# Kernel tuning notes

Measured on AMD Instinct MI355X. Metric: run time of the kernel, lower is better.

The kernel has to match this reference:

```python
import jax, jax.numpy as jnp
import numpy as np

B, S, H, HD, WIN, KS = 2, 2048, 8, 64, 64, 2048
D = H * HD          # slotsize = nheads * headsize = 512
SUB = 1 + 2 * WIN   # window length = 129
LN_EPS = 1e-3       # Keras LayerNormalization default epsilon


def setup_inputs() -> dict:
    key = jax.random.key(0)
    ks = jax.random.split(key, 5)
    s = 0.02
    return {
        "values": jax.random.normal(ks[0], (B, S, D), jnp.float32),
        "W_kqv": jax.random.normal(ks[1], (D, 3 * D), jnp.float32) * s,
        "b_kqv": jnp.zeros((3 * D,), jnp.float32),
        "ln_gamma": jnp.ones((D,), jnp.float32),
        "ln_beta": jnp.zeros((D,), jnp.float32),
        "W_kernel": jax.random.normal(ks[2], (D, KS), jnp.float32) * s,
        "b_kernel": jnp.zeros((KS,), jnp.float32),
        "W_proj": jax.random.normal(ks[3], (KS, D), jnp.float32) * s,
        "b_proj": jnp.zeros((D,), jnp.float32),
    }


def _layernorm(x, g, b):
    mu = jnp.mean(x, axis=-1, keepdims=True)
    var = jnp.var(x, axis=-1, keepdims=True)
    return (x - mu) * jax.lax.rsqrt(var + LN_EPS) * g + b


def reference(values, W_kqv, b_kqv, ln_gamma, ln_beta, W_kernel, b_kernel, W_proj, b_proj):
    # fused qkv projection: [B,S,3D]
    kqv = values @ W_kqv + b_kqv
    k, q, v = jnp.split(kqv, 3, axis=2)
    # shared layernorm applied to q and k (over full D)
    q = _layernorm(q, ln_gamma, ln_beta)
    k = _layernorm(k, ln_gamma, ln_beta)
    kh = k.reshape(B, S, H, HD)
    qh = q.reshape(B, S, H, HD)
    vh = v.reshape(B, S, H, HD)
    starts = jnp.clip(jnp.arange(S) - WIN, 0, S - SUB)
    idx = starts[:, None] + jnp.arange(SUB)          # [S, SUB]
    kw = kh[:, idx]                                  # [B,S,SUB,H,HD]
    vw = vh[:, idx]                                  # [B,S,SUB,H,HD]
    scores = jnp.einsum('bshd,bswhd->bshw', qh, kw) / np.float32(np.sqrt(HD))
    attn = jax.nn.softmax(scores, axis=-1)           # [B,S,H,SUB]
    ctx = jnp.einsum('bshw,bswhd->bshd', attn, vw).reshape(B, S, D)
    # residual MLP (dropout rate 0 -> identity)
    x = jax.nn.relu(ctx @ W_kernel + b_kernel)
    x = x @ W_proj + b_proj
    return x + v  # residual is the value projection, per the original code
```

## Files before the change

### kernel.cpp

```cpp
#include <hip/hip_runtime.h>
#include <hip/hip_bf16.h>

#define B_ 2
#define S_ 2048
#define H_ 8
#define HD_ 64
#define WIN_ 64
#define SUB_ 129
#define D_ 512
#define KS_ 2048
#define M_ 4096
#define LN_EPS 1e-3f

typedef unsigned short u16;
typedef short bf16x8 __attribute__((ext_vector_type(8)));
typedef float f32x4 __attribute__((ext_vector_type(4)));

__device__ inline u16 f2bf(float x) {
  unsigned int u = __float_as_uint(x);
  return (u16)((u + 0x7fffu + ((u >> 16) & 1u)) >> 16);
}
__device__ inline float bf2f(u16 u) {
  return __uint_as_float(((unsigned int)u) << 16);
}
__device__ inline float bf2f_lo(unsigned int u) { return __uint_as_float(u << 16); }
__device__ inline float bf2f_hi(unsigned int u) { return __uint_as_float(u & 0xffff0000u); }

__device__ inline void gll16(const u16* g, u16* l) {
  __builtin_amdgcn_global_load_lds(
      (const __attribute__((address_space(1))) void*)g,
      (__attribute__((address_space(3))) void*)l, 16, 0, 0);
}

template <int EPI>
__global__ __launch_bounds__(256) void mfma_gemm(
    const u16* __restrict__ A, const u16* __restrict__ Bt,
    const float* __restrict__ bias, u16* __restrict__ Cout,
    float* __restrict__ stats, int K, int lda, int ldb, int ldc, int TN) {
  __shared__ __align__(16) u16 As[2][8192];
  __shared__ __align__(16) u16 Bs[2][8192];

  const int tid = threadIdx.x;
  const int wv = tid >> 6;
  const int ln = tid & 63;

  const int id = blockIdx.x;
  const int xcd = id & 7;
  const int sub = id >> 3;
  const int tn = sub % TN;
  const int msub = sub / TN;
  const int row0 = (xcd * 4 + msub) << 7;
  const int col0 = tn << 7;

  const int lrow = ln >> 3;
  const int lchunk = (ln & 7) ^ lrow;
  const u16* ag = A + (size_t)(row0 + 32 * wv + lrow) * lda + lchunk * 8;
  const u16* bg = Bt + (size_t)(col0 + 32 * wv + lrow) * ldb + lchunk * 8;
  const int lbase = 32 * wv * 64;

  const int quad = ln >> 4;
  const int l15 = ln & 15;
  const int r7 = l15 & 7;
  const int wm = (wv & 1) << 6;
  const int wn = (wv >> 1) << 6;

  f32x4 acc[4][4];
#pragma unroll
  for (int i = 0; i < 4; ++i)
#pragma unroll
    for (int j = 0; j < 4; ++j) acc[i][j] = (f32x4){0.f, 0.f, 0.f, 0.f};

#define STAGE(buf, koff)                                            \
  do {                                                              \
    const u16* a0 = ag + (koff);                                    \
    const u16* b0 = bg + (koff);                                    \
    u16* la = &As[buf][lbase];                                      \
    u16* lb = &Bs[buf][lbase];                                      \
    gll16(a0, la);                                                  \
    gll16(a0 + 8 * (size_t)lda, la + 512);                          \
    gll16(a0 + 16 * (size_t)lda, la + 1024);                       \
    gll16(a0 + 24 * (size_t)lda, la + 1536);                       \
    gll16(b0, lb);                                                  \
    gll16(b0 + 8 * (size_t)ldb, lb + 512);                          \
    gll16(b0 + 16 * (size_t)ldb, lb + 1024);                       \
    gll16(b0 + 24 * (size_t)ldb, lb + 1536);                       \
  } while (0)

  const int nk = K >> 6;
  STAGE(0, 0);

  for (int ki = 0; ki < nk; ++ki) {
    __syncthreads();
    if (ki + 1 < nk) STAGE((ki + 1) & 1, (ki + 1) << 6);

    const char* Ab = (const char*)As[ki & 1];
    const char* Bb = (const char*)Bs[ki & 1];
#pragma unroll
    for (int ks = 0; ks < 2; ++ks) {
      const int pc = ((quad + 4 * ks) ^ r7) << 4;
      bf16x8 af[4], bfv[4];
#pragma unroll
      for (int mi = 0; mi < 4; ++mi)
        af[mi] = *(const bf16x8*)(Ab + (wm + 16 * mi + l15) * 128 + pc);
#pragma unroll
      for (int ni = 0; ni < 4; ++ni)
        bfv[ni] = *(const bf16x8*)(Bb + (wn + 16 * ni + l15) * 128 + pc);
#pragma unroll
      for (int mi = 0; mi < 4; ++mi)
#pragma unroll
        for (int ni = 0; ni < 4; ++ni)
          acc[mi][ni] = __builtin_amdgcn_mfma_f32_16x16x32_bf16(
              bfv[ni], af[mi], acc[mi][ni], 0, 0, 0);
    }
  }
#undef STAGE

  const int c00 = col0 + wn + (quad << 2);
  float4 bv[4];
#pragma unroll
  for (int ni = 0; ni < 4; ++ni) bv[ni] = *(const float4*)&bias[c00 + ni * 16];

#pragma unroll
  for (int mi = 0; mi < 4; ++mi) {
    const int row = row0 + wm + 16 * mi + l15;
    float s = 0.f, ss = 0.f;
#pragma unroll
    for (int ni = 0; ni < 4; ++ni) {
      float v0 = acc[mi][ni][0] + bv[ni].x;
      float v1 = acc[mi][ni][1] + bv[ni].y;
      float v2 = acc[mi][ni][2] + bv[ni].z;
      float v3 = acc[mi][ni][3] + bv[ni].w;
      if (EPI == 1) {
        v0 = fmaxf(v0, 0.f); v1 = fmaxf(v1, 0.f);
        v2 = fmaxf(v2, 0.f); v3 = fmaxf(v3, 0.f);
      }
      if (EPI == 3) {
        s += v0 + v1 + v2 + v3;
        ss += v0 * v0 + v1 * v1 + v2 * v2 + v3 * v3;
      }
      ushort4 o = {f2bf(v0), f2bf(v1), f2bf(v2), f2bf(v3)};
      *(ushort4*)&Cout[(size_t)row * ldc + c00 + ni * 16] = o;
    }
    if (EPI == 3) {
      s += __shfl_xor(s, 16); ss += __shfl_xor(ss, 16);
      s += __shfl_xor(s, 32); ss += __shfl_xor(ss, 32);
      if (quad == 0 && col0 < 1024) {
        const int half = col0 >> 9;
        atomicAdd(&stats[(size_t)row * 4 + half * 2 + 0], s);
        atomicAdd(&stats[(size_t)row * 4 + half * 2 + 1], ss);
      }
    }
  }
}

__global__ __launch_bounds__(256) void mfma_gemm64(
    const u16* __restrict__ A, const u16* __restrict__ Bt,
    const float* __restrict__ bias, const u16* __restrict__ extra,
    float* __restrict__ Cout, int K, int lda, int ldb, int ldc, int eld) {
  __shared__ __align__(16) u16 As[2][4096];
  __shared__ __align__(16) u16 Bs[2][4096];

  const int tid = threadIdx.x;
  const int wv = tid >> 6;
  const int ln = tid & 63;

  const int id = blockIdx.x;
  const int xcd = id & 7;
  const int sub = id >> 3;
  const int tn = sub & 7;
  const int msub = sub >> 3;
  const int row0 = (xcd * 8 + msub) << 6;
  const int col0 = tn << 6;

  const int lrow = ln >> 3;
  const int lchunk = (ln & 7) ^ lrow;
  const u16* ag = A + (size_t)(row0 + 16 * wv + lrow) * lda + lchunk * 8;
  const u16* bg = Bt + (size_t)(col0 + 16 * wv + lrow) * ldb + lchunk * 8;
  const int lbase = 16 * wv * 64;

  const int quad = ln >> 4;
  const int l15 = ln & 15;
  const int r7 = l15 & 7;
  const int wm = (wv & 1) << 5;
  const int wn = (wv >> 1) << 5;

  f32x4 acc[2][2];
#pragma unroll
  for (int i = 0; i < 2; ++i)
#pragma unroll
    for (int j = 0; j < 2; ++j) acc[i][j] = (f32x4){0.f, 0.f, 0.f, 0.f};

#define STAGE64(buf, koff)                                          \
  do {                                                              \
    const u16* a0 = ag + (koff);                                    \
    const u16* b0 = bg + (koff);                                    \
    u16* la = &As[buf][lbase];                                      \
    u16* lb = &Bs[buf][lbase];                                      \
    gll16(a0, la);                                                  \
    gll16(a0 + 8 * (size_t)lda, la + 512);                          \
    gll16(b0, lb);                                                  \
    gll16(b0 + 8 * (size_t)ldb, lb + 512);                          \
  } while (0)

  const int nk = K >> 6;
  STAGE64(0, 0);

  for (int ki = 0; ki < nk; ++ki) {
    __syncthreads();
    if (ki + 1 < nk) STAGE64((ki + 1) & 1, (ki + 1) << 6);

    const char* Ab = (const char*)As[ki & 1];
    const char* Bb = (const char*)Bs[ki & 1];
#pragma unroll
    for (int ks = 0; ks < 2; ++ks) {
      const int pc = ((quad + 4 * ks) ^ r7) << 4;
      bf16x8 af[2], bfv[2];
#pragma unroll
      for (int mi = 0; mi < 2; ++mi)
        af[mi] = *(const bf16x8*)(Ab + (wm + 16 * mi + l15) * 128 + pc);
#pragma unroll
      for (int ni = 0; ni < 2; ++ni)
        bfv[ni] = *(const bf16x8*)(Bb + (wn + 16 * ni + l15) * 128 + pc);
#pragma unroll
      for (int mi = 0; mi < 2; ++mi)
#pragma unroll
        for (int ni = 0; ni < 2; ++ni)
          acc[mi][ni] = __builtin_amdgcn_mfma_f32_16x16x32_bf16(
              bfv[ni], af[mi], acc[mi][ni], 0, 0, 0);
    }
  }
#undef STAGE64

  const int c00 = col0 + wn + (quad << 2);
  float4 bv[2];
#pragma unroll
  for (int ni = 0; ni < 2; ++ni) bv[ni] = *(const float4*)&bias[c00 + ni * 16];

#pragma unroll
  for (int mi = 0; mi < 2; ++mi) {
    const int row = row0 + wm + 16 * mi + l15;
#pragma unroll
    for (int ni = 0; ni < 2; ++ni) {
      const int c = c00 + ni * 16;
      uint2 ex = *(const uint2*)&extra[(size_t)row * eld + c];
      float4 o;
      o.x = acc[mi][ni][0] + bv[ni].x + bf2f_lo(ex.x);
      o.y = acc[mi][ni][1] + bv[ni].y + bf2f_hi(ex.x);
      o.z = acc[mi][ni][2] + bv[ni].z + bf2f_lo(ex.y);
      o.w = acc[mi][ni][3] + bv[ni].w + bf2f_hi(ex.y);
      *(float4*)&Cout[(size_t)row * ldc + c] = o;
    }
  }
}

__global__ __launch_bounds__(256) void fused_cvt(
    const float* __restrict__ values, u16* __restrict__ vals_bf,
    const float* __restrict__ Wkqv, u16* __restrict__ wkqv_t,
    const float* __restrict__ Wker, u16* __restrict__ wker_t,
    const float* __restrict__ Wproj, u16* __restrict__ wproj_t,
    float* __restrict__ stats) {
  __shared__ float t[32][33];
  const int id = blockIdx.x;
  if (id >= 3840) {
    const int i = ((id - 3840) * 256 + threadIdx.x) * 4;
    *(float4*)&stats[i] = (float4){0.f, 0.f, 0.f, 0.f};
    return;
  }
  if (id < 1024) {
    const int i = (id * 256 + threadIdx.x) * 8;
    float4 a = *(const float4*)&values[i];
    float4 b = *(const float4*)&values[i + 4];
    union { u16 u[8]; uint4 v; } pk;
    pk.u[0] = f2bf(a.x); pk.u[1] = f2bf(a.y); pk.u[2] = f2bf(a.z); pk.u[3] = f2bf(a.w);
    pk.u[4] = f2bf(b.x); pk.u[5] = f2bf(b.y); pk.u[6] = f2bf(b.z); pk.u[7] = f2bf(b.w);
    *(uint4*)&vals_bf[i] = pk.v;
    return;
  }
  const float* W; u16* Wt; int K, N, nx, lin;
  if (id < 1792)      { lin = id - 1024; W = Wkqv;  Wt = wkqv_t;  K = 512;  N = 1536; nx = 48; }
  else if (id < 2816) { lin = id - 1792; W = Wker;  Wt = wker_t;  K = 512;  N = 2048; nx = 64; }
  else                { lin = id - 2816; W = Wproj; Wt = wproj_t; K = 2048; N = 512;  nx = 16; }
  const int n0 = (lin % nx) << 5;
  const int k0 = (lin / nx) << 5;
  const int r = threadIdx.x >> 3;
  const int c4 = (threadIdx.x & 7) << 2;
  float4 v = *(const float4*)&W[(size_t)(k0 + r) * N + n0 + c4];
  t[r][c4 + 0] = v.x; t[r][c4 + 1] = v.y; t[r][c4 + 2] = v.z; t[r][c4 + 3] = v.w;
  __syncthreads();
  ushort4 o;
  o.x = f2bf(t[c4 + 0][r]); o.y = f2bf(t[c4 + 1][r]);
  o.z = f2bf(t[c4 + 2][r]); o.w = f2bf(t[c4 + 3][r]);
  *(ushort4*)&Wt[(size_t)(n0 + r) * K + k0 + c4] = o;
}

__global__ __launch_bounds__(256) void attn_kernel(
    const u16* __restrict__ kqv, const float* __restrict__ stats,
    const float* __restrict__ gamma, const float* __restrict__ beta,
    u16* __restrict__ ctx) {
  __shared__ __align__(16) u16 Ks[192 * 64];
  __shared__ __align__(16) u16 Vt[64 * 192];
  __shared__ __align__(16) u16 Ps[4 * 16 * 192];
  __shared__ float kr[192], km[192];
  __shared__ float qm[64], qr[64];
  __shared__ float g1[64], b1[64];

  const int bid = blockIdx.x;
  const int tile = bid & 31;
  const int h = (bid >> 5) & 7;
  const int b = bid >> 8;
  const int t0 = tile << 6;

  int g0 = t0 - WIN_;
  if (g0 < 0) g0 = 0;
  if (g0 > S_ - SUB_) g0 = S_ - SUB_;

  const int tid = threadIdx.x;
  const int wv = tid >> 6;
  const int ln = tid & 63;
  const size_t rowb = (size_t)(b * S_);

  {
    const int krow = ln >> 3;
    const int kch = (ln & 7) ^ krow;
#pragma unroll
    for (int it = 0; it < 6; ++it) {
      const int kb = it * 32 + wv * 8;
      gll16(&kqv[(rowb + g0 + kb + krow) * 1536 + h * 64 + kch * 8],
            &Ks[kb * 64]);
    }
  }
  if (tid < 192) {
    const size_t rr = rowb + g0 + tid;
    const float s = stats[rr * 4 + 0], ss = stats[rr * 4 + 1];
    const float mu = s * (1.f / 512.f);
    const float var = ss * (1.f / 512.f) - mu * mu;
    const float rs = rsqrtf(var + LN_EPS);
    kr[tid] = rs * 0.125f;
    km[tid] = mu * rs * 0.125f;
  } else {
    const int t = tid - 192;
    const size_t rr = rowb + t0 + t;
    const float s = stats[rr * 4 + 2], ss = stats[rr * 4 + 3];
    const float mu = s * (1.f / 512.f);
    const float var = ss * (1.f / 512.f) - mu * mu;
    qm[t] = mu;
    qr[t] = rsqrtf(var + LN_EPS);
  }
#pragma unroll
  for (int it = 0; it < 12; ++it) {
    const int item = tid + it * 256;
    const int dg = item / 192;
    const int key = item - dg * 192;
    uint2 v = *(const uint2*)&kqv[(rowb + g0 + key) * 1536 + 1024 + h * 64 + dg * 4];
    const int c = key >> 3;
    u16 e[4] = {(u16)(v.x & 0xffff), (u16)(v.x >> 16),
                (u16)(v.y & 0xffff), (u16)(v.y >> 16)};
#pragma unroll
    for (int j = 0; j < 4; ++j) {
      const int d = dg * 4 + j;
      const int phys = (c & 24) | ((c ^ d) & 7);
      Vt[d * 192 + phys * 8 + (key & 7)] = e[j];
    }
  }
  __syncthreads();

#pragma unroll
  for (int it = 0; it < 2; ++it) {
    const int item = tid + it * 256;
    const int qq = item >> 3, c = item & 7;
    const int phys = c ^ (qq & 7);
    uint4 v = *(const uint4*)&kqv[(rowb + t0 + qq) * 1536 + 512 + h * 64 + c * 8];
    const float mu = qm[qq], rs = qr[qq];
    union { float4 f4[2]; float f[8]; } gl, bl;
    gl.f4[0] = *(const float4*)&gamma[h * 64 + c * 8];
    gl.f4[1] = *(const float4*)&gamma[h * 64 + c * 8 + 4];
    bl.f4[0] = *(const float4*)&beta[h * 64 + c * 8];
    bl.f4[1] = *(const float4*)&beta[h * 64 + c * 8 + 4];
    const float x[8] = {bf2f_lo(v.x), bf2f_hi(v.x), bf2f_lo(v.y), bf2f_hi(v.y),
                        bf2f_lo(v.z), bf2f_hi(v.z), bf2f_lo(v.w), bf2f_hi(v.w)};
    float g1p = 0.f, b1p = 0.f;
    union { u16 u[8]; uint4 v; } pk;
#pragma unroll
    for (int j = 0; j < 8; ++j) {
      const float qp = (x[j] - mu) * rs * gl.f[j] + bl.f[j];
      const u16 qg = f2bf(qp * gl.f[j]);
      pk.u[j] = qg;
      g1p += bf2f(qg);
      b1p += qp * bl.f[j];
    }
    g1p += __shfl_xor(g1p, 1); b1p += __shfl_xor(b1p, 1);
    g1p += __shfl_xor(g1p, 2); b1p += __shfl_xor(b1p, 2);
    g1p += __shfl_xor(g1p, 4); b1p += __shfl_xor(b1p, 4);
    if ((tid & 7) == 0) { g1[qq] = g1p; b1[qq] = b1p * 0.125f; }
    *(uint4*)&Ps[qq * 64 + phys * 8] = pk.v;
  }
  __syncthreads();

  const int quad = ln >> 4;
  const int l15 = ln & 15;
  const int l7 = l15 & 7;
  const int qbase = wv << 4;

  bf16x8 qf[2];
#pragma unroll
  for (int ks = 0; ks < 2; ++ks) {
    const int phys = (ks * 4 + quad) ^ l7;
    qf[ks] = *(const bf16x8*)&Ps[(qbase + l15) * 64 + phys * 8];
  }

  f32x4 sacc[12];
#pragma unroll
  for (int nt = 0; nt < 12; ++nt) sacc[nt] = (f32x4){0.f, 0.f, 0.f, 0.f};
#pragma unroll
  for (int ks = 0; ks < 2; ++ks) {
    const int phys = (ks * 4 + quad) ^ l7;
#pragma unroll
    for (int nt = 0; nt < 12; ++nt) {
      bf16x8 kf = *(const bf16x8*)&Ks[(nt * 16 + l15) * 64 + phys * 8];
      sacc[nt] = __builtin_amdgcn_mfma_f32_16x16x32_bf16(qf[ks], kf, sacc[nt], 0, 0, 0);
    }
  }

  int off[4];
  float g1m[4], b1s[4];
#pragma unroll
  for (int r = 0; r < 4; ++r) {
    const int qg = t0 + qbase + quad * 4 + r;
    int st = qg - WIN_;
    if (st < 0) st = 0;
    if (st > S_ - SUB_) st = S_ - SUB_;
    off[r] = st - g0;
    g1m[r] = g1[qbase + quad * 4 + r];
    b1s[r] = b1[qbase + quad * 4 + r];
  }

  float rmax[4] = {-1e30f, -1e30f, -1e30f, -1e30f};
#pragma unroll
  for (int nt = 0; nt < 12; ++nt) {
    const int n = nt * 16 + l15;
    const float rsn = kr[n], mn = km[n];
#pragma unroll
    for (int r = 0; r < 4; ++r) {
      const bool valid = (n >= off[r]) && (n < off[r] + SUB_);
      const float sv = fmaf(rsn, sacc[nt][r], fmaf(-mn, g1m[r], b1s[r]));
      const float v = valid ? sv : -1e30f;
      sacc[nt][r] = v;
      rmax[r] = fmaxf(rmax[r], v);
    }
  }
#pragma unroll
  for (int m = 1; m < 16; m <<= 1)
#pragma unroll
    for (int r = 0; r < 4; ++r) rmax[r] = fmaxf(rmax[r], __shfl_xor(rmax[r], m));

  float rsum[4] = {0.f, 0.f, 0.f, 0.f};
#pragma unroll
  for (int nt = 0; nt < 12; ++nt) {
#pragma unroll
    for (int r = 0; r < 4; ++r) {
      const float e = __expf(sacc[nt][r] - rmax[r]);
      sacc[nt][r] = e;
      rsum[r] += e;
    }
  }
#pragma unroll
  for (int m = 1; m < 16; m <<= 1)
#pragma unroll
    for (int r = 0; r < 4; ++r) rsum[r] += __shfl_xor(rsum[r], m);
  float inv[4];
#pragma unroll
  for (int r = 0; r < 4; ++r) inv[r] = 1.f / rsum[r];

  __syncthreads();

  u16* psw = &Ps[wv * 16 * 192];
#pragma unroll
  for (int nt = 0; nt < 12; ++nt) {
    const int n = nt * 16 + l15;
    const int c = n >> 3;
#pragma unroll
    for (int r = 0; r < 4; ++r) {
      const int m = quad * 4 + r;
      const int phys = (c & 24) | ((c ^ m) & 7);
      psw[m * 192 + phys * 8 + (n & 7)] = f2bf(sacc[nt][r]);
    }
  }
  __syncthreads();

  f32x4 oacc[4];
#pragma unroll
  for (int nt = 0; nt < 4; ++nt) oacc[nt] = (f32x4){0.f, 0.f, 0.f, 0.f};
#pragma unroll
  for (int ks = 0; ks < 6; ++ks) {
    const int c = ks * 4 + quad;
    const int phys = (c & 24) | ((c ^ l7) & 7);
    bf16x8 pf = *(const bf16x8*)&psw[l15 * 192 + phys * 8];
#pragma unroll
    for (int nt = 0; nt < 4; ++nt) {
      bf16x8 vf = *(const bf16x8*)&Vt[(nt * 16 + l15) * 192 + phys * 8];
      oacc[nt] = __builtin_amdgcn_mfma_f32_16x16x32_bf16(pf, vf, oacc[nt], 0, 0, 0);
    }
  }

#pragma unroll
  for (int nt = 0; nt < 4; ++nt) {
#pragma unroll
    for (int r = 0; r < 4; ++r) {
      const int row = t0 + qbase + quad * 4 + r;
      const int col = h * 64 + nt * 16 + l15;
      ctx[(rowb + row) * D_ + col] = f2bf(oacc[nt][r] * inv[r]);
    }
  }
}

extern "C" void kernel_launch(void* const* d_in, const int* in_sizes, int n_in,
                              void* d_out, int out_size, void* d_ws,
                              size_t ws_size, hipStream_t stream) {
  (void)in_sizes; (void)n_in; (void)out_size; (void)ws_size;
  const float* values   = (const float*)d_in[0];
  const float* W_kqv    = (const float*)d_in[1];
  const float* b_kqv    = (const float*)d_in[2];
  const float* ln_gamma = (const float*)d_in[3];
  const float* ln_beta  = (const float*)d_in[4];
  const float* W_kernel = (const float*)d_in[5];
  const float* b_kernel = (const float*)d_in[6];
  const float* W_proj   = (const float*)d_in[7];
  const float* b_proj   = (const float*)d_in[8];
  float* out = (float*)d_out;

  u16* kqv     = (u16*)d_ws;
  u16* vals_bf = kqv + (size_t)M_ * 1536;
  u16* ctx_bf  = vals_bf + (size_t)M_ * 512;
  u16* x_bf    = ctx_bf + (size_t)M_ * 512;
  u16* wkqv_t  = x_bf + (size_t)M_ * 2048;
  u16* wker_t  = wkqv_t + (size_t)1536 * 512;
  u16* wproj_t = wker_t + (size_t)2048 * 512;
  float* stats = (float*)(wproj_t + (size_t)512 * 2048);

  fused_cvt<<<3857, 256, 0, stream>>>(values, vals_bf, W_kqv, wkqv_t,
                                      W_kernel, wker_t, W_proj, wproj_t,
                                      stats);

  mfma_gemm<3><<<384, 256, 0, stream>>>(
      vals_bf, wkqv_t, b_kqv, kqv, stats, 512, 512, 512, 1536, 12);

  attn_kernel<<<B_ * H_ * (S_ / 64), 256, 0, stream>>>(
      kqv, stats, ln_gamma, ln_beta, ctx_bf);

  mfma_gemm<1><<<512, 256, 0, stream>>>(
      ctx_bf, wker_t, b_kernel, x_bf, nullptr, 512, 512, 512, KS_, 16);

  mfma_gemm64<<<512, 256, 0, stream>>>(
      x_bf, wproj_t, b_proj, kqv + 1024, out, KS_, KS_, KS_, D_, 1536);
}
```

Measured before the change: 151.6 us.

## Use 128x96 tiles for QKV GEMM to fill all CUs; widen V transpose loads

Adds a dedicated QKV-projection GEMM with 128x96 output tiles, so the launch grows from 384 to 512 blocks. That gives a more even wave count across the compute units of the MI355X. Because a 96-wide tile can span the k/q boundary, the LayerNorm statistics epilogue now keeps separate k and q sums and does per-half atomics. The attention kernel's V transpose now loads 8 bf16 values per thread instead of 4, halving the number of global load iterations. The risks are smaller per-block reuse, more atomics, and wave-level mixing of halves.

```diff
diff --git a/kernel.cpp b/kernel.cpp
--- a/kernel.cpp
+++ b/kernel.cpp
@@ -35,8 +35,8 @@
 template <int EPI>
 __global__ __launch_bounds__(256) void mfma_gemm(
     const u16* __restrict__ A, const u16* __restrict__ Bt,
-    const float* __restrict__ bias, u16* __restrict__ Cout,
-    float* __restrict__ stats, int K, int lda, int ldb, int ldc, int TN) {
+    const float* __restrict__ bias, u16* __restrict__ Cout, int K, int lda,
+    int ldb, int ldc, int TN) {
   __shared__ __align__(16) u16 As[2][8192];
   __shared__ __align__(16) u16 Bs[2][8192];
 
@@ -123,7 +123,6 @@
 #pragma unroll
   for (int mi = 0; mi < 4; ++mi) {
     const int row = row0 + wm + 16 * mi + l15;
-    float s = 0.f, ss = 0.f;
 #pragma unroll
     for (int ni = 0; ni < 4; ++ni) {
       float v0 = acc[mi][ni][0] + bv[ni].x;
@@ -134,20 +133,139 @@
         v0 = fmaxf(v0, 0.f); v1 = fmaxf(v1, 0.f);
         v2 = fmaxf(v2, 0.f); v3 = fmaxf(v3, 0.f);
       }
-      if (EPI == 3) {
-        s += v0 + v1 + v2 + v3;
-        ss += v0 * v0 + v1 * v1 + v2 * v2 + v3 * v3;
+      ushort4 o = {f2bf(v0), f2bf(v1), f2bf(v2), f2bf(v3)};
+      *(ushort4*)&Cout[(size_t)row * ldc + c00 + ni * 16] = o;
+    }
+  }
+}
+
+__global__ __launch_bounds__(256) void mfma_gemm96(
+    const u16* __restrict__ A, const u16* __restrict__ Bt,
+    const float* __restrict__ bias, u16* __restrict__ Cout,
+    float* __restrict__ stats, int K, int lda, int ldb, int ldc) {
+  __shared__ __align__(16) u16 As[2][8192];
+  __shared__ __align__(16) u16 Bs[2][6144];
+
+  const int tid = threadIdx.x;
+  const int wv = tid >> 6;
+  const int ln = tid & 63;
+
+  const int id = blockIdx.x;
+  const int xcd = id & 7;
+  const int sub = id >> 3;
+  const int tn = sub & 15;
+  const int msub = sub >> 4;
+  const int row0 = (xcd * 4 + msub) << 7;
+  const int col0 = tn * 96;
+
+  const int lrow = ln >> 3;
+  const int lchunk = (ln & 7) ^ lrow;
+  const u16* ag = A + (size_t)(row0 + 32 * wv + lrow) * lda + lchunk * 8;
+  const u16* bg = Bt + (size_t)(col0 + 24 * wv + lrow) * ldb + lchunk * 8;
+
+  const int quad = ln >> 4;
+  const int l15 = ln & 15;
+  const int r7 = l15 & 7;
+  const int wm = (wv & 1) << 6;
+  const int wn = (wv >> 1) * 48;
+
+  f32x4 acc[4][3];
+#pragma unroll
+  for (int i = 0; i < 4; ++i)
+#pragma unroll
+    for (int j = 0; j < 3; ++j) acc[i][j] = (f32x4){0.f, 0.f, 0.f, 0.f};
+
+#define STAGE96(buf, koff)                                          \
+  do {                                                              \
+    const u16* a0 = ag + (koff);                                    \
+    const u16* b0 = bg + (koff);                                    \
+    u16* la = &As[buf][2048 * wv];                                  \
+    u16* lb = &Bs[buf][1536 * wv];                                  \
+    gll16(a0, la);                                                  \
+    gll16(a0 + 8 * (size_t)lda, la + 512);                          \
+    gll16(a0 + 16 * (size_t)lda, la + 1024);                       \
+    gll16(a0 + 24 * (size_t)lda, la + 1536);                       \
+    gll16(b0, lb);                                                  \
+    gll16(b0 + 8 * (size_t)ldb, lb + 512);                          \
+    gll16(b0 + 16 * (size_t)ldb, lb + 1024);                       \
+  } while (0)
+
+  const int nk = K >> 6;
+  STAGE96(0, 0);
+
+  for (int ki = 0; ki < nk; ++ki) {
+    __syncthreads();
+    if (ki + 1 < nk) STAGE96((ki + 1) & 1, (ki + 1) << 6);
+
+    const char* Ab = (const char*)As[ki & 1];
+    const char* Bb = (const char*)Bs[ki & 1];
+#pragma unroll
+    for (int ks = 0; ks < 2; ++ks) {
+      const int pc = ((quad + 4 * ks) ^ r7) << 4;
+      bf16x8 af[4], bfv[3];
+#pragma unroll
+      for (int mi = 0; mi < 4; ++mi)
+        af[mi] = *(const bf16x8*)(Ab + (wm + 16 * mi + l15) * 128 + pc);
+#pragma unroll
+      for (int ni = 0; ni < 3; ++ni)
+        bfv[ni] = *(const bf16x8*)(Bb + (wn + 16 * ni + l15) * 128 + pc);
+#pragma unroll
+      for (int mi = 0; mi < 4; ++mi)
+#pragma unroll
+        for (int ni = 0; ni < 3; ++ni)
+          acc[mi][ni] = __builtin_amdgcn_mfma_f32_16x16x32_bf16(
+              bfv[ni], af[mi], acc[mi][ni], 0, 0, 0);
+    }
+  }
+#undef STAGE96
+
+  const int c00 = col0 + wn + (quad << 2);
+  float4 bv[3];
+  int half[3];
+  bool hk = false, hq = false;
+#pragma unroll
+  for (int ni = 0; ni < 3; ++ni) {
+    bv[ni] = *(const float4*)&bias[c00 + ni * 16];
+    const int cb = col0 + wn + ni * 16;
+    half[ni] = cb >> 9;
+    if (half[ni] == 0) hk = true;
+    if (half[ni] == 1) hq = true;
+  }
+
+#pragma unroll
+  for (int mi = 0; mi < 4; ++mi) {
+    const int row = row0 + wm + 16 * mi + l15;
+    float sk = 0.f, ssk = 0.f, sq = 0.f, ssq = 0.f;
+#pragma unroll
+    for (int ni = 0; ni < 3; ++ni) {
+      float v0 = acc[mi][ni][0] + bv[ni].x;
+      float v1 = acc[mi][ni][1] + bv[ni].y;
+      float v2 = acc[mi][ni][2] + bv[ni].z;
+      float v3 = acc[mi][ni][3] + bv[ni].w;
+      if (half[ni] == 0) {
+        sk += v0 + v1 + v2 + v3;
+        ssk += v0 * v0 + v1 * v1 + v2 * v2 + v3 * v3;
+      } else if (half[ni] == 1) {
+        sq += v0 + v1 + v2 + v3;
+        ssq += v0 * v0 + v1 * v1 + v2 * v2 + v3 * v3;
       }
       ushort4 o = {f2bf(v0), f2bf(v1), f2bf(v2), f2bf(v3)};
       *(ushort4*)&Cout[(size_t)row * ldc + c00 + ni * 16] = o;
     }
-    if (EPI == 3) {
-      s += __shfl_xor(s, 16); ss += __shfl_xor(ss, 16);
-      s += __shfl_xor(s, 32); ss += __shfl_xor(ss, 32);
-      if (quad == 0 && col0 < 1024) {
-        const int half = col0 >> 9;
-        atomicAdd(&stats[(size_t)row * 4 + half * 2 + 0], s);
-        atomicAdd(&stats[(size_t)row * 4 + half * 2 + 1], ss);
+    if (hk) {
+      sk += __shfl_xor(sk, 16); ssk += __shfl_xor(ssk, 16);
+      sk += __shfl_xor(sk, 32); ssk += __shfl_xor(ssk, 32);
+      if (quad == 0) {
+        atomicAdd(&stats[(size_t)row * 4 + 0], sk);
+        atomicAdd(&stats[(size_t)row * 4 + 1], ssk);
+      }
+    }
+    if (hq) {
+      sq += __shfl_xor(sq, 16); ssq += __shfl_xor(ssq, 16);
+      sq += __shfl_xor(sq, 32); ssq += __shfl_xor(ssq, 32);
+      if (quad == 0) {
+        atomicAdd(&stats[(size_t)row * 4 + 2], sq);
+        atomicAdd(&stats[(size_t)row * 4 + 3], ssq);
       }
     }
   }
@@ -347,19 +465,18 @@
     qr[t] = rsqrtf(var + LN_EPS);
   }
 #pragma unroll
-  for (int it = 0; it < 12; ++it) {
+  for (int it = 0; it < 6; ++it) {
     const int item = tid + it * 256;
-    const int dg = item / 192;
-    const int key = item - dg * 192;
-    uint2 v = *(const uint2*)&kqv[(rowb + g0 + key) * 1536 + 1024 + h * 64 + dg * 4];
+    const int dg8 = item / 192;
+    const int key = item - dg8 * 192;
+    union { uint4 v; u16 u[8]; } uu;
+    uu.v = *(const uint4*)&kqv[(rowb + g0 + key) * 1536 + 1024 + h * 64 + dg8 * 8];
     const int c = key >> 3;
-    u16 e[4] = {(u16)(v.x & 0xffff), (u16)(v.x >> 16),
-                (u16)(v.y & 0xffff), (u16)(v.y >> 16)};
-#pragma unroll
-    for (int j = 0; j < 4; ++j) {
-      const int d = dg * 4 + j;
+#pragma unroll
+    for (int j = 0; j < 8; ++j) {
+      const int d = dg8 * 8 + j;
       const int phys = (c & 24) | ((c ^ d) & 7);
-      Vt[d * 192 + phys * 8 + (key & 7)] = e[j];
+      Vt[d * 192 + phys * 8 + (key & 7)] = uu.u[j];
     }
   }
   __syncthreads();
@@ -541,14 +658,14 @@
                                       W_kernel, wker_t, W_proj, wproj_t,
                                       stats);
 
-  mfma_gemm<3><<<384, 256, 0, stream>>>(
-      vals_bf, wkqv_t, b_kqv, kqv, stats, 512, 512, 512, 1536, 12);
+  mfma_gemm96<<<512, 256, 0, stream>>>(
+      vals_bf, wkqv_t, b_kqv, kqv, stats, 512, 512, 512, 1536);
 
   attn_kernel<<<B_ * H_ * (S_ / 64), 256, 0, stream>>>(
       kqv, stats, ln_gamma, ln_beta, ctx_bf);
 
   mfma_gemm<1><<<512, 256, 0, stream>>>(
-      ctx_bf, wker_t, b_kernel, x_bf, nullptr, 512, 512, 512, KS_, 16);
+      ctx_bf, wker_t, b_kernel, x_bf, 512, 512, 512, KS_, 16);
 
   mfma_gemm64<<<512, 256, 0, stream>>>(
       x_bf, wproj_t, b_proj, kqv + 1024, out, KS_, KS_, KS_, D_, 1536);
```

Result: no change. 151.5 us (-0.1%).
